# Kernel tuning notes

Measured on AMD Instinct MI355X. Metric: run time of the kernel, lower is better.

## Reference

```python
import jax, jax.numpy as jnp
import numpy as np

B, T, C, H, DH, L, V = 16, 1023, 384, 6, 64, 6, 256
FF = 4 * C
EPS = 1e-5


def _ln(x, g, b):
    mu = x.mean(-1, keepdims=True)
    var = ((x - mu) ** 2).mean(-1, keepdims=True)
    return (x - mu) * jax.lax.rsqrt(var + EPS) * g + b


def setup_inputs() -> dict:
    key = jax.random.key(0)
    ks = jax.random.split(key, 12)
    n = lambda k, shp: jax.random.normal(k, shp, dtype=jnp.float32) * 0.02
    return {
        "x": jax.random.randint(ks[0], (B, T), 0, V),
        "targets": jax.random.randint(ks[1], (B, T), 0, V),
        "tok_emb": n(ks[2], (V, C)),
        "pos_emb": n(ks[3], (T, C)),
        "Wq": n(ks[4], (L, C, C)), "Wk": n(ks[5], (L, C, C)), "Wv": n(ks[6], (L, C, C)),
        "Wo": n(ks[7], (L, C, C)), "bo": jnp.zeros((L, C)),
        "ln1_g": jnp.ones((L, C)), "ln1_b": jnp.zeros((L, C)),
        "ln2_g": jnp.ones((L, C)), "ln2_b": jnp.zeros((L, C)),
        "W1": n(ks[8], (L, C, FF)), "b1": jnp.zeros((L, FF)),
        "W2": n(ks[9], (L, FF, C)), "b2": jnp.zeros((L, C)),
        "lnf_g": jnp.ones((C,)), "lnf_b": jnp.zeros((C,)),
        "Wf": n(ks[10], (C, V)), "bf": jnp.zeros((V,)),
    }


def _forward(x, targets, tok_emb, pos_emb, Wq, Wk, Wv, Wo, bo,
             ln1_g, ln1_b, ln2_g, ln2_b, W1, b1, W2, b2, lnf_g, lnf_b, Wf, bf):
    h = tok_emb[x] + pos_emb[None, :, :]  # [B,T,C]
    tril = jnp.tril(jnp.ones((T, T), bool))

    def heads(z, W):  # [B,T,C] @ [C,C] -> [B,H,T,DH]
        return jnp.einsum('btc,cd->btd', z, W).reshape(B, T, H, DH).transpose(0, 2, 1, 3)

    def layer(h, p):
        wq, wk, wv, wo, bo_, g1, be1, g2, be2, w1, bb1, w2, bb2 = p
        z = _ln(h, g1, be1)
        q, k, v = heads(z, wq), heads(z, wk), heads(z, wv)
        qk = jnp.einsum('bhtd,bhsd->bhts', q, k) * (DH ** -0.5)
        zm = jnp.where(tril, qk, 0.0)
        # faithful to torch: masked_fill_(zeromask == 0, -inf)
        zm = jnp.where(zm == 0.0, -jnp.inf, zm)
        att = jax.nn.softmax(zm, axis=-1)  # dropout = identity (eval)
        o = jnp.einsum('bhts,bhsd->bhtd', att, v).transpose(0, 2, 1, 3).reshape(B, T, C)
        h = h + jnp.einsum('btc,cd->btd', o, wo) + bo_
        z2 = _ln(h, g2, be2)
        ff = jax.nn.relu(jnp.einsum('btc,cf->btf', z2, w1) + bb1)
        h = h + jnp.einsum('btf,fc->btc', ff, w2) + bb2
        return h, None

    params = (Wq, Wk, Wv, Wo, bo, ln1_g, ln1_b, ln2_g, ln2_b, W1, b1, W2, b2)
    h, _ = jax.lax.scan(layer, h, params)
    logits = jnp.einsum('btc,cv->btv', _ln(h, lnf_g, lnf_b), Wf) + bf
    logits2 = logits.reshape(B * T, V)
    logp = jax.nn.log_softmax(logits2, axis=-1)
    loss = -jnp.take_along_axis(logp, targets.reshape(B * T, 1), axis=1).mean()
    return logits2, loss


def reference(x, targets, tok_emb, pos_emb, Wq, Wk, Wv, Wo, bo,
              ln1_g, ln1_b, ln2_g, ln2_b, W1, b1, W2, b2, lnf_g, lnf_b, Wf, bf):
    return _forward(x, targets, tok_emb, pos_emb, Wq, Wk, Wv, Wo, bo,
                    ln1_g, ln1_b, ln2_g, ln2_b, W1, b1, W2, b2, lnf_g, lnf_b, Wf, bf)
```

## Files before the change

kernel.cpp:

```cpp
#include <hip/hip_runtime.h>
#include <hip/hip_bf16.h>
#include <math.h>

#define B_  16
#define T_  1023
#define C_  384
#define H_  6
#define DH_ 64
#define L_  6
#define V_  256
#define FF_ 1536
#define M_  (B_*T_)
#define MP_ 16384
#define EPS_ 1e-5f

typedef __attribute__((ext_vector_type(8))) short bf16x8;
typedef __attribute__((ext_vector_type(4))) short short4v;
typedef __attribute__((ext_vector_type(4))) float f32x4;

__device__ inline short f2bf(float x) {
    union { float f; unsigned u; } c; c.f = x;
    unsigned r = (c.u + 0x7fffu + ((c.u >> 16) & 1u)) >> 16;
    return (short)r;
}

#define GLDS16(g, l) __builtin_amdgcn_global_load_lds(                         \
    (const __attribute__((address_space(1))) void*)(g),                        \
    (__attribute__((address_space(3))) void*)(l), 16, 0, 0)

#define TRRD(dst, va, IMM) asm volatile("ds_read_b64_tr_b16 %0, %1 offset:" IMM \
    : "=v"(dst) : "v"(va))

__global__ void embed_kernel(const int* __restrict__ x, const float* __restrict__ tok,
                             const float* __restrict__ pos, float* __restrict__ h) {
    int i = blockIdx.x * 256 + threadIdx.x;
    if (i >= M_ * C_) return;
    int bt = i / C_;
    int c  = i - bt * C_;
    int t  = bt % T_;
    h[i] = tok[x[bt] * C_ + c] + pos[t * C_ + c];
}

__global__ __launch_bounds__(256) void wconv_kernel(
    const float* __restrict__ Wq, const float* __restrict__ Wk,
    const float* __restrict__ Wv, const float* __restrict__ Wo,
    const float* __restrict__ W1, const float* __restrict__ W2,
    const float* __restrict__ Wf,
    short* __restrict__ qkvt, short* __restrict__ wot, short* __restrict__ w1t,
    short* __restrict__ w2t, short* __restrict__ wft) {
    __shared__ float tile[32][33];
    int t = blockIdx.x;
    const float* src; short* dst; int K, N, tl;
    if (t < 10368) {
        int l = t / 1728, r = t - l * 1728;
        if (r < 432) {
            int which = r / 144; tl = r - which * 144;
            src = (which == 0 ? Wq : which == 1 ? Wk : Wv) + (size_t)l * 384 * 384;
            dst = qkvt + (size_t)l * 1152 * 384 + (size_t)which * 384 * 384;
            K = 384; N = 384;
        } else if (r < 576) {
            tl = r - 432;
            src = Wo + (size_t)l * 384 * 384; dst = wot + (size_t)l * 384 * 384;
            K = 384; N = 384;
        } else if (r < 1152) {
            tl = r - 576;
            src = W1 + (size_t)l * 384 * 1536; dst = w1t + (size_t)l * 1536 * 384;
            K = 384; N = 1536;
        } else {
            tl = r - 1152;
            src = W2 + (size_t)l * 1536 * 384; dst = w2t + (size_t)l * 384 * 1536;
            K = 1536; N = 384;
        }
    } else {
        tl = t - 10368; src = Wf; dst = wft; K = 384; N = 256;
    }
    int ntx = N >> 5;
    int k0 = (tl / ntx) << 5, n0 = (tl % ntx) << 5;
    int rr = threadIdx.x >> 5, cc = threadIdx.x & 31;
#pragma unroll
    for (int p = 0; p < 4; ++p)
        tile[rr + 8 * p][cc] = src[(size_t)(k0 + rr + 8 * p) * N + n0 + cc];
    __syncthreads();
#pragma unroll
    for (int p = 0; p < 4; ++p)
        dst[(size_t)(n0 + rr + 8 * p) * K + k0 + cc] = f2bf(tile[cc][rr + 8 * p]);
}

__global__ __launch_bounds__(256) void ln_kernel(const float* __restrict__ in,
                                                 const float* __restrict__ g,
                                                 const float* __restrict__ b,
                                                 short* __restrict__ out) {
    int wave = threadIdx.x >> 6, lane = threadIdx.x & 63;
    int row  = blockIdx.x * 4 + wave;
    const float* rp = in + (size_t)row * C_;
    float v[6];
    float s = 0.f, s2 = 0.f;
#pragma unroll
    for (int i = 0; i < 6; ++i) {
        v[i] = rp[i * 64 + lane];
        s  += v[i];
        s2 += v[i] * v[i];
    }
#pragma unroll
    for (int o = 32; o > 0; o >>= 1) {
        s  += __shfl_xor(s,  o, 64);
        s2 += __shfl_xor(s2, o, 64);
    }
    float mu  = s * (1.0f / C_);
    float var = s2 * (1.0f / C_) - mu * mu;
    float rs  = rsqrtf(var + EPS_);
    short* op = out + (size_t)row * C_;
#pragma unroll
    for (int i = 0; i < 6; ++i) {
        int c = i * 64 + lane;
        op[c] = f2bf((v[i] - mu) * rs * g[c] + b[c]);
    }
}

template<int MODE, bool RELU, bool HB>
__global__ __launch_bounds__(256) void mm_kernel(const short* __restrict__ A,
                                                 const short* __restrict__ Bt,
                                                 const float* __restrict__ bias,
                                                 short* __restrict__ outb,
                                                 float* __restrict__ outf,
                                                 int N, int K) {
    __shared__ short Al[2][8][128][8];
    __shared__ short Bl[2][8][128][8];
    int tid  = threadIdx.x;
    int wave = tid >> 6, lane = tid & 63;
    int kg4 = lane >> 4, r16 = lane & 15;
    int wr = (wave >> 1) * 64, wc = (wave & 1) * 64;
    int row0 = blockIdx.x * 128, col0 = blockIdx.y * 128;

    const short* ga = A  + (size_t)(row0 + (tid & 127)) * K + ((tid >> 7) << 5);
    const short* gb = Bt + (size_t)(col0 + (tid & 127)) * K + ((tid >> 7) << 5);
    short* alds = &Al[0][0][0][0];
    short* blds = &Bl[0][0][0][0];
    int ldst = ((tid >> 7) << 2) * 1024 + (tid & 127) * 8;

    f32x4 acc[4][4];
#pragma unroll
    for (int i = 0; i < 4; ++i)
#pragma unroll
        for (int j = 0; j < 4; ++j) { acc[i][j][0]=0.f; acc[i][j][1]=0.f; acc[i][j][2]=0.f; acc[i][j][3]=0.f; }

#define MM_STAGE(BUF)                                                          \
    {                                                                          \
        short* la = alds + (BUF) * 8192 + ldst;                                \
        short* lb = blds + (BUF) * 8192 + ldst;                                \
        GLDS16(ga,      la);        GLDS16(ga + 8,  la + 1024);                \
        GLDS16(ga + 16, la + 2048); GLDS16(ga + 24, la + 3072);                \
        GLDS16(gb,      lb);        GLDS16(gb + 8,  lb + 1024);                \
        GLDS16(gb + 16, lb + 2048); GLDS16(gb + 24, lb + 3072);                \
        ga += 64; gb += 64;                                                    \
    }

#define MM_COMPUTE(BUF)                                                        \
    {                                                                          \
        _Pragma("unroll")                                                      \
        for (int p = 0; p < 2; ++p) {                                          \
            const short* ab = alds + (BUF) * 8192 + (4 * p + kg4) * 1024;      \
            const short* bb = blds + (BUF) * 8192 + (4 * p + kg4) * 1024;      \
            bf16x8 av[4], bv[4];                                               \
            _Pragma("unroll")                                                  \
            for (int i = 0; i < 4; ++i) av[i] = *(const bf16x8*)(ab + (wr + 16*i + r16) * 8); \
            _Pragma("unroll")                                                  \
            for (int j = 0; j < 4; ++j) bv[j] = *(const bf16x8*)(bb + (wc + 16*j + r16) * 8); \
            _Pragma("unroll")                                                  \
            for (int i = 0; i < 4; ++i)                                        \
                _Pragma("unroll")                                              \
                for (int j = 0; j < 4; ++j)                                    \
                    acc[i][j] = __builtin_amdgcn_mfma_f32_16x16x32_bf16(av[i], bv[j], acc[i][j], 0, 0, 0); \
        }                                                                      \
    }

    int NT = K >> 6;
    MM_STAGE(0);
    MM_STAGE(1);
    asm volatile("s_waitcnt vmcnt(8)" ::: "memory");
    __builtin_amdgcn_s_barrier();
    asm volatile("" ::: "memory");

    for (int t = 0; t < NT - 1; ++t) {
        MM_COMPUTE(t & 1);
        __builtin_amdgcn_s_barrier();
        asm volatile("" ::: "memory");
        if (t + 2 < NT) {
            MM_STAGE(t & 1);
            asm volatile("s_waitcnt vmcnt(8)" ::: "memory");
        } else {
            asm volatile("s_waitcnt vmcnt(0)" ::: "memory");
        }
        __builtin_amdgcn_s_barrier();
        asm volatile("" ::: "memory");
    }
    MM_COMPUTE((NT - 1) & 1);
#undef MM_STAGE
#undef MM_COMPUTE

#pragma unroll
    for (int j = 0; j < 4; ++j) {
        int col = col0 + wc + 16 * j + r16;
        float bj = HB ? bias[col] : 0.f;
#pragma unroll
        for (int i = 0; i < 4; ++i) {
#pragma unroll
            for (int rg = 0; rg < 4; ++rg) {
                int row = row0 + wr + 16 * i + 4 * kg4 + rg;
                float v = acc[i][j][rg] + bj;
                if (RELU) v = fmaxf(v, 0.f);
                if (MODE == 0) {
                    outb[(size_t)row * N + col] = f2bf(v);
                } else if (MODE == 1) {
                    outf[(size_t)row * N + col] += v;
                } else {
                    if (row < M_) outf[(size_t)row * N + col] = v;
                }
            }
        }
    }
}

__global__ __launch_bounds__(512) void ffn_kernel(const short* zin,
                                                  const short* __restrict__ w1t,
                                                  const short* __restrict__ w2t,
                                                  const float* __restrict__ b1,
                                                  const float* __restrict__ b2,
                                                  float* __restrict__ h,
                                                  const float* __restrict__ lng,
                                                  const float* __restrict__ lnb,
                                                  short* zout) {
    __shared__ short Zl[48 * 64 * 8];
    __shared__ short Pl[16 * 64 * 8];
    int tid  = threadIdx.x;
    int wave = tid >> 6, lane = tid & 63;
    int g = lane >> 4, r16 = lane & 15;
    int r0 = blockIdx.x * 64;

    {
        const short* gz = zin + (size_t)(r0 + lane) * C_ + wave * 8;
        short* lz = Zl + (wave * 64 + lane) * 8;
#pragma unroll
        for (int ro = 0; ro < 6; ++ro) {
            GLDS16(gz, lz);
            gz += 64;
            lz += 8 * 64 * 8;
        }
    }

    const short* w1base = w1t + (size_t)(16 * wave + r16) * C_ + 8 * g;
    const short* w2base = w2t + (size_t)(48 * wave + r16) * FF_ + 8 * g;

    bf16x8 w1f[12];
#pragma unroll
    for (int ks = 0; ks < 12; ++ks)
        w1f[ks] = *(const bf16x8*)(w1base + ks * 32);

    asm volatile("s_waitcnt vmcnt(0)" ::: "memory");
    __builtin_amdgcn_s_barrier();
    asm volatile("" ::: "memory");

    f32x4 acc2[4][3];
#pragma unroll
    for (int mi = 0; mi < 4; ++mi)
#pragma unroll
        for (int j = 0; j < 3; ++j) { acc2[mi][j][0]=0.f; acc2[mi][j][1]=0.f; acc2[mi][j][2]=0.f; acc2[mi][j][3]=0.f; }

    for (int c = 0; c < 12; ++c) {
        bf16x8 w2f[12];
#pragma unroll
        for (int ks2 = 0; ks2 < 4; ++ks2)
#pragma unroll
            for (int j = 0; j < 3; ++j)
                w2f[ks2 * 3 + j] = *(const bf16x8*)(w2base + (size_t)(16 * j) * FF_
                                                    + 128 * c + 32 * ks2);

        f32x4 acc1[4];
#pragma unroll
        for (int mj = 0; mj < 4; ++mj) { acc1[mj][0]=0.f; acc1[mj][1]=0.f; acc1[mj][2]=0.f; acc1[mj][3]=0.f; }
#pragma unroll
        for (int ks = 0; ks < 12; ++ks) {
#pragma unroll
            for (int mj = 0; mj < 4; ++mj) {
                bf16x8 bz = *(const bf16x8*)(Zl + ((4 * ks + g) * 64 + 16 * mj + r16) * 8);
                acc1[mj] = __builtin_amdgcn_mfma_f32_16x16x32_bf16(w1f[ks], bz, acc1[mj], 0, 0, 0);
            }
        }
        f32x4 b1v = *(const f32x4*)(b1 + 128 * c + 16 * wave + 4 * g);
        int oct = 2 * wave + (g >> 1);
#pragma unroll
        for (int mj = 0; mj < 4; ++mj) {
            short4v pv;
#pragma unroll
            for (int rg = 0; rg < 4; ++rg)
                pv[rg] = f2bf(fmaxf(acc1[mj][rg] + b1v[rg], 0.f));
            *(short4v*)(Pl + (oct * 64 + 16 * mj + r16) * 8 + (g & 1) * 4) = pv;
        }
        __syncthreads();

        if (c + 1 < 12) {
#pragma unroll
            for (int ks = 0; ks < 12; ++ks)
                w1f[ks] = *(const bf16x8*)(w1base + (size_t)(c + 1) * 128 * C_ + ks * 32);
        }

#pragma unroll
        for (int ks2 = 0; ks2 < 4; ++ks2) {
            bf16x8 pa[4];
#pragma unroll
            for (int mi = 0; mi < 4; ++mi)
                pa[mi] = *(const bf16x8*)(Pl + ((4 * ks2 + g) * 64 + 16 * mi + r16) * 8);
#pragma unroll
            for (int j = 0; j < 3; ++j) {
#pragma unroll
                for (int mi = 0; mi < 4; ++mi)
                    acc2[mi][j] = __builtin_amdgcn_mfma_f32_16x16x32_bf16(pa[mi], w2f[ks2 * 3 + j], acc2[mi][j], 0, 0, 0);
            }
        }
        __syncthreads();
    }

    float rsum[4][4], rsq[4][4];
#pragma unroll
    for (int mi = 0; mi < 4; ++mi)
#pragma unroll
        for (int rg = 0; rg < 4; ++rg) { rsum[mi][rg] = 0.f; rsq[mi][rg] = 0.f; }

#pragma unroll
    for (int j = 0; j < 3; ++j) {
        int col = 48 * wave + 16 * j + r16;
        float bj = b2[col];
#pragma unroll
        for (int mi = 0; mi < 4; ++mi) {
#pragma unroll
            for (int rg = 0; rg < 4; ++rg) {
                int row = r0 + 16 * mi + 4 * g + rg;
                float hv = h[(size_t)row * C_ + col] + acc2[mi][j][rg] + bj;
                h[(size_t)row * C_ + col] = hv;
                acc2[mi][j][rg] = hv;
                rsum[mi][rg] += hv;
                rsq[mi][rg]  += hv * hv;
            }
        }
    }
#pragma unroll
    for (int o = 1; o < 16; o <<= 1) {
#pragma unroll
        for (int mi = 0; mi < 4; ++mi)
#pragma unroll
            for (int rg = 0; rg < 4; ++rg) {
                rsum[mi][rg] += __shfl_xor(rsum[mi][rg], o, 64);
                rsq[mi][rg]  += __shfl_xor(rsq[mi][rg],  o, 64);
            }
    }
    float* St = (float*)Pl;
    if (r16 == 0) {
#pragma unroll
        for (int mi = 0; mi < 4; ++mi)
#pragma unroll
            for (int rg = 0; rg < 4; ++rg) {
                int rr = 16 * mi + 4 * g + rg;
                St[rr * 16 + 2 * wave]     = rsum[mi][rg];
                St[rr * 16 + 2 * wave + 1] = rsq[mi][rg];
            }
    }
    __syncthreads();
    if (tid < 64) {
        float s = 0.f, s2 = 0.f;
#pragma unroll
        for (int w = 0; w < 8; ++w) { s += St[tid * 16 + 2 * w]; s2 += St[tid * 16 + 2 * w + 1]; }
        float mu  = s * (1.0f / C_);
        float var = s2 * (1.0f / C_) - mu * mu;
        St[tid * 16]     = mu;
        St[tid * 16 + 1] = rsqrtf(var + EPS_);
    }
    __syncthreads();
#pragma unroll
    for (int j = 0; j < 3; ++j) {
        int col = 48 * wave + 16 * j + r16;
        float gam = lng[col], bet = lnb[col];
#pragma unroll
        for (int mi = 0; mi < 4; ++mi) {
#pragma unroll
            for (int rg = 0; rg < 4; ++rg) {
                int rr = 16 * mi + 4 * g + rg;
                float mu = St[rr * 16], rs = St[rr * 16 + 1];
                zout[(size_t)(r0 + rr) * C_ + col] = f2bf((acc2[mi][j][rg] - mu) * rs * gam + bet);
            }
        }
    }
}

__device__ __forceinline__ void attn_step(int kt, int qg, int g, int r16,
                                          const char* Kb, unsigned ka, unsigned va,
                                          short (*Pw)[40],
                                          bf16x8 qf0, bf16x8 qf1,
                                          f32x4* o_acc, float& m, float& l) {
    f32x4 s0, s1;
    s0[0]=0.f;s0[1]=0.f;s0[2]=0.f;s0[3]=0.f;
    s1[0]=0.f;s1[1]=0.f;s1[2]=0.f;s1[3]=0.f;
    bf16x8 a00 = *(const bf16x8*)(Kb + ka);
    bf16x8 a01 = *(const bf16x8*)(Kb + (ka ^ 64u));
    bf16x8 a10 = *(const bf16x8*)(Kb + ka + 2048u);
    bf16x8 a11 = *(const bf16x8*)(Kb + ((ka + 2048u) ^ 64u));
    s0 = __builtin_amdgcn_mfma_f32_16x16x32_bf16(a00, qf0, s0, 0, 0, 0);
    s0 = __builtin_amdgcn_mfma_f32_16x16x32_bf16(a01, qf1, s0, 0, 0, 0);
    s1 = __builtin_amdgcn_mfma_f32_16x16x32_bf16(a10, qf0, s1, 0, 0, 0);
    s1 = __builtin_amdgcn_mfma_f32_16x16x32_bf16(a11, qf1, s1, 0, 0, 0);

    int kb0 = kt * 32 + 4 * g;
    float sv[8];
#pragma unroll
    for (int r = 0; r < 4; ++r) {
        sv[r]     = (kb0 + r      <= qg) ? s0[r] * 0.125f : -3e38f;
        sv[4 + r] = (kb0 + 16 + r <= qg) ? s1[r] * 0.125f : -3e38f;
    }
    float pmax = sv[0];
#pragma unroll
    for (int i = 1; i < 8; ++i) pmax = fmaxf(pmax, sv[i]);
    pmax = fmaxf(pmax, __shfl_xor(pmax, 16, 64));
    pmax = fmaxf(pmax, __shfl_xor(pmax, 32, 64));
    float mn   = fmaxf(m, pmax);
    float corr = __expf(m - mn);
    float rs = 0.f;
    short pb[8];
#pragma unroll
    for (int i = 0; i < 8; ++i) {
        float p = __expf(sv[i] - mn);
        rs += p;
        pb[i] = f2bf(p);
    }
    rs += __shfl_xor(rs, 16, 64);
    rs += __shfl_xor(rs, 32, 64);
    l = l * corr + rs;
    m = mn;

    short4v t0w, t1w;
    t0w[0]=pb[0]; t0w[1]=pb[1]; t0w[2]=pb[2]; t0w[3]=pb[3];
    t1w[0]=pb[4]; t1w[1]=pb[5]; t1w[2]=pb[6]; t1w[3]=pb[7];
    *(short4v*)&Pw[r16][4 * g]      = t0w;
    *(short4v*)&Pw[r16][16 + 4 * g] = t1w;

    short4v v0, v1, v2, v3, v4, v5, v6, v7;
    TRRD(v0, va, "0");    TRRD(v1, va, "512");
    TRRD(v2, va, "128");  TRRD(v3, va, "640");
    TRRD(v4, va, "256");  TRRD(v5, va, "768");
    TRRD(v6, va, "384");  TRRD(v7, va, "896");

    bf16x8 pB = *(const bf16x8*)&Pw[r16][8 * g];
#pragma unroll
    for (int d = 0; d < 4; ++d) {
        o_acc[d][0] *= corr; o_acc[d][1] *= corr;
        o_acc[d][2] *= corr; o_acc[d][3] *= corr;
    }
    asm volatile("s_waitcnt lgkmcnt(0)" ::: "memory");
    __builtin_amdgcn_sched_barrier(0);

    bf16x8 av0, av1, av2, av3;
#pragma unroll
    for (int i = 0; i < 4; ++i) {
        av0[i] = v0[i]; av0[i + 4] = v1[i];
        av1[i] = v2[i]; av1[i + 4] = v3[i];
        av2[i] = v4[i]; av2[i + 4] = v5[i];
        av3[i] = v6[i]; av3[i + 4] = v7[i];
    }
    o_acc[0] = __builtin_amdgcn_mfma_f32_16x16x32_bf16(av0, pB, o_acc[0], 0, 0, 0);
    o_acc[1] = __builtin_amdgcn_mfma_f32_16x16x32_bf16(av1, pB, o_acc[1], 0, 0, 0);
    o_acc[2] = __builtin_amdgcn_mfma_f32_16x16x32_bf16(av2, pB, o_acc[2], 0, 0, 0);
    o_acc[3] = __builtin_amdgcn_mfma_f32_16x16x32_bf16(av3, pB, o_acc[3], 0, 0, 0);
}

__global__ __launch_bounds__(256) void attn_kernel(const short* __restrict__ qkv,
                                                   short* __restrict__ o) {
    __shared__ short Kl[32 * 64];
    __shared__ short Vl[32 * 64];
    __shared__ short P_lds[4][16][40];

    int tid  = threadIdx.x;
    int wave = tid >> 6;
    int lane = tid & 63;
    int g    = lane >> 4;
    int r16  = lane & 15;

    int qtA = blockIdx.x;
    int qtB = 15 - qtA;
    int bh = blockIdx.y;
    int b  = bh / H_, hh = bh - b * H_;
    size_t rbase = (size_t)b * T_;
    int qoff = hh * 64;

    int q0A = qtA * 64, q0B = qtB * 64;
    int qgA = q0A + wave * 16 + r16;
    int qgB = q0B + wave * 16 + r16;

    const short* qrA = qkv + (rbase + qgA) * 1152 + qoff;
    const short* qrB = qkv + (rbase + qgB) * 1152 + qoff;
    bf16x8 qfA0 = *(const bf16x8*)(qrA + 8 * g);
    bf16x8 qfA1 = *(const bf16x8*)(qrA + 32 + 8 * g);
    bf16x8 qfB0 = *(const bf16x8*)(qrB + 8 * g);
    bf16x8 qfB1 = *(const bf16x8*)(qrB + 32 + 8 * g);

    int kkey = tid >> 3;
    int koct = (tid & 7) ^ (kkey & 7);
    const short* gk = qkv + (rbase + kkey) * 1152 + qoff + 384 + koct * 8;
    int vkey = 4 * (tid >> 5) + ((tid >> 1) & 3);
    int voct = 2 * ((tid >> 3) & 3) + (tid & 1);
    const short* gv = qkv + (rbase + vkey) * 1152 + qoff + 768 + voct * 8;
    short* lk = Kl + tid * 8;
    short* lv = Vl + tid * 8;

    f32x4 oA[4], oB[4];
#pragma unroll
    for (int d = 0; d < 4; ++d) {
        oA[d][0]=0.f; oA[d][1]=0.f; oA[d][2]=0.f; oA[d][3]=0.f;
        oB[d][0]=0.f; oB[d][1]=0.f; oB[d][2]=0.f; oB[d][3]=0.f;
    }
    float mA = -3e38f, lA = 0.f, mB = -3e38f, lB = 0.f;

    const char* Kb = (const char*)Kl;
    unsigned ka = (unsigned)(r16 * 128 + ((g ^ (r16 & 7)) << 4));
    unsigned va = (unsigned)(size_t)(__attribute__((address_space(3))) short*)Vl
                + 1024u * (unsigned)g + 8u * (unsigned)r16;

    int ktA_hi = (q0A + wave * 16 + 15) >> 5;
    int ktB_hi = (q0B + wave * 16 + 15) >> 5;
    int nkt = 2 * (qtB + 1);

    for (int kt = 0; kt < nkt; ++kt) {
        __syncthreads();
        GLDS16(gk, lk);
        GLDS16(gv, lv);
        gk += 32 * 1152; gv += 32 * 1152;
        __syncthreads();

        if (kt <= ktB_hi)
            attn_step(kt, qgB, g, r16, Kb, ka, va, P_lds[wave], qfB0, qfB1, oB, mB, lB);
        if (kt <= ktA_hi)
            attn_step(kt, qgA, g, r16, Kb, ka, va, P_lds[wave], qfA0, qfA1, oA, mA, lA);
    }

    {
        float inv = (lA > 0.f) ? 1.f / lA : 0.f;
        short* orow = o + (rbase + qgA) * C_ + qoff;
#pragma unroll
        for (int d = 0; d < 4; ++d) {
            short4v ov;
#pragma unroll
            for (int r = 0; r < 4; ++r) ov[r] = f2bf(oA[d][r] * inv);
            *(short4v*)(orow + 16 * d + 4 * g) = ov;
        }
    }
    if (qgB < T_) {
        float inv = (lB > 0.f) ? 1.f / lB : 0.f;
        short* orow = o + (rbase + qgB) * C_ + qoff;
#pragma unroll
        for (int d = 0; d < 4; ++d) {
            short4v ov;
#pragma unroll
            for (int r = 0; r < 4; ++r) ov[r] = f2bf(oB[d][r] * inv);
            *(short4v*)(orow + 16 * d + 4 * g) = ov;
        }
    }
}

__global__ __launch_bounds__(64) void nll_kernel(const float* __restrict__ logits,
                                                 const int* __restrict__ tgt,
                                                 float* __restrict__ nll) {
    int row  = blockIdx.x;
    int lane = threadIdx.x;
    const float* rp = logits + (size_t)row * V_;
    float v[4];
    float mx = -INFINITY;
#pragma unroll
    for (int i = 0; i < 4; ++i) {
        v[i] = rp[i * 64 + lane];
        mx = fmaxf(mx, v[i]);
    }
#pragma unroll
    for (int o = 32; o > 0; o >>= 1) mx = fmaxf(mx, __shfl_xor(mx, o, 64));
    float s = 0.f;
#pragma unroll
    for (int i = 0; i < 4; ++i) s += expf(v[i] - mx);
#pragma unroll
    for (int o = 32; o > 0; o >>= 1) s += __shfl_xor(s, o, 64);
    if (lane == 0) {
        float lse = mx + logf(s);
        nll[row] = lse - rp[tgt[row]];
    }
}

__global__ __launch_bounds__(256) void loss_kernel(const float* __restrict__ nll,
                                                   float* __restrict__ loss) {
    __shared__ float sm[256];
    float s = 0.f;
    for (int i = threadIdx.x; i < M_; i += 256) s += nll[i];
    sm[threadIdx.x] = s;
    __syncthreads();
    for (int o = 128; o > 0; o >>= 1) {
        if (threadIdx.x < o) sm[threadIdx.x] += sm[threadIdx.x + o];
        __syncthreads();
    }
    if (threadIdx.x == 0) *loss = sm[0] * (1.0f / M_);
}

extern "C" void kernel_launch(void* const* d_in, const int* in_sizes, int n_in,
                              void* d_out, int out_size, void* d_ws, size_t ws_size,
                              hipStream_t stream) {
    const int*   x       = (const int*)d_in[0];
    const int*   targets = (const int*)d_in[1];
    const float* tok_emb = (const float*)d_in[2];
    const float* pos_emb = (const float*)d_in[3];
    const float* Wq      = (const float*)d_in[4];
    const float* Wk      = (const float*)d_in[5];
    const float* Wv      = (const float*)d_in[6];
    const float* Wo      = (const float*)d_in[7];
    const float* bo      = (const float*)d_in[8];
    const float* ln1_g   = (const float*)d_in[9];
    const float* ln1_b   = (const float*)d_in[10];
    const float* ln2_g   = (const float*)d_in[11];
    const float* ln2_b   = (const float*)d_in[12];
    const float* W1      = (const float*)d_in[13];
    const float* b1      = (const float*)d_in[14];
    const float* W2      = (const float*)d_in[15];
    const float* b2      = (const float*)d_in[16];
    const float* lnf_g   = (const float*)d_in[17];
    const float* lnf_b   = (const float*)d_in[18];
    const float* Wf      = (const float*)d_in[19];
    const float* bf      = (const float*)d_in[20];

    float* logits = (float*)d_out;
    float* loss   = logits + (size_t)M_ * V_;

    float* h    = (float*)d_ws;
    short* z    = (short*)(h + (size_t)MP_ * C_);
    short* big  = z + (size_t)MP_ * C_;
    short* ob   = big + (size_t)MP_ * FF_;
    short* qkvt = ob + (size_t)MP_ * C_;
    short* wot  = qkvt + (size_t)L_ * 1152 * 384;
    short* w1t  = wot + (size_t)L_ * 384 * 384;
    short* w2t  = w1t + (size_t)L_ * 1536 * 384;
    short* wft  = w2t + (size_t)L_ * 1536 * 384;
    float* nll  = (float*)(wft + (size_t)256 * 384);

    wconv_kernel<<<10464, 256, 0, stream>>>(Wq, Wk, Wv, Wo, W1, W2, Wf,
                                            qkvt, wot, w1t, w2t, wft);
    embed_kernel<<<(M_ * C_ + 255) / 256, 256, 0, stream>>>(x, tok_emb, pos_emb, h);

    for (int l = 0; l < L_; ++l) {
        if (l == 0)
            ln_kernel<<<M_ / 4, 256, 0, stream>>>(h, ln1_g, ln1_b, z);
        mm_kernel<0, false, false><<<dim3(128, 9), 256, 0, stream>>>(
            z, qkvt + (size_t)l * 1152 * 384, nullptr, big, nullptr, 1152, 384);
        attn_kernel<<<dim3(8, B_ * H_), 256, 0, stream>>>(big, ob);
        mm_kernel<1, false, true><<<dim3(128, 3), 256, 0, stream>>>(
            ob, wot + (size_t)l * 384 * 384, bo + l * C_, nullptr, h, 384, 384);
        ln_kernel<<<M_ / 4, 256, 0, stream>>>(h, ln2_g + l * C_, ln2_b + l * C_, z);
        const float* ng = (l + 1 < L_) ? ln1_g + (l + 1) * C_ : lnf_g;
        const float* nb = (l + 1 < L_) ? ln1_b + (l + 1) * C_ : lnf_b;
        ffn_kernel<<<MP_ / 64, 512, 0, stream>>>(
            z, w1t + (size_t)l * 1536 * 384, w2t + (size_t)l * 384 * 1536,
            b1 + l * FF_, b2 + l * C_, h, ng, nb, z);
    }

    mm_kernel<2, false, true><<<dim3(128, 2), 256, 0, stream>>>(
        z, wft, bf, nullptr, logits, 256, 384);

    nll_kernel<<<M_, 64, 0, stream>>>(logits, targets, nll);
    loss_kernel<<<1, 256, 0, stream>>>(nll, loss);
}
```

Before: 1.323 ms.

## Software-pipeline FFN kernel with double-buffered hidden activations in LDS

Restructures the fused FFN loop so the second GEMM for chunk c runs before the first GEMM for chunk c+1. The hidden activations are double-buffered in shared memory, which removes one of the two barriers per iteration. W1 and W2 weight loads are issued one stage ahead so global latency can overlap MFMA work. It uses twice the LDS for the hidden buffer and may raise register pressure from keeping both weight fragment sets live.

```diff
diff --git a/kernel.cpp b/kernel.cpp
--- a/kernel.cpp
+++ b/kernel.cpp
@@ -231,7 +231,7 @@
                                                   const float* __restrict__ lnb,
                                                   short* zout) {
     __shared__ short Zl[48 * 64 * 8];
-    __shared__ short Pl[16 * 64 * 8];
+    __shared__ short Pl[2][16 * 64 * 8];
     int tid  = threadIdx.x;
     int wave = tid >> 6, lane = tid & 63;
     int g = lane >> 4, r16 = lane & 15;
@@ -251,74 +251,101 @@
     const short* w1base = w1t + (size_t)(16 * wave + r16) * C_ + 8 * g;
     const short* w2base = w2t + (size_t)(48 * wave + r16) * FF_ + 8 * g;
 
-    bf16x8 w1f[12];
-#pragma unroll
-    for (int ks = 0; ks < 12; ++ks)
-        w1f[ks] = *(const bf16x8*)(w1base + ks * 32);
-
+    bf16x8 w1f[12], w2f[12];
+    f32x4 acc1[4];
+    f32x4 acc2[4][3];
+
+#define W1LOAD(cc)                                                             \
+    {                                                                          \
+        _Pragma("unroll")                                                      \
+        for (int ks = 0; ks < 12; ++ks)                                        \
+            w1f[ks] = *(const bf16x8*)(w1base + (size_t)(cc) * 128 * C_ + ks * 32); \
+    }
+
+#define W2LOAD(cc)                                                             \
+    {                                                                          \
+        _Pragma("unroll")                                                      \
+        for (int ks2 = 0; ks2 < 4; ++ks2)                                      \
+            _Pragma("unroll")                                                  \
+            for (int j = 0; j < 3; ++j)                                        \
+                w2f[ks2 * 3 + j] = *(const bf16x8*)(w2base + (size_t)(16 * j) * FF_ \
+                                                    + 128 * (cc) + 32 * ks2);  \
+    }
+
+#define FF1C()                                                                 \
+    {                                                                          \
+        _Pragma("unroll")                                                      \
+        for (int mj = 0; mj < 4; ++mj) { acc1[mj][0]=0.f; acc1[mj][1]=0.f; acc1[mj][2]=0.f; acc1[mj][3]=0.f; } \
+        _Pragma("unroll")                                                      \
+        for (int ks = 0; ks < 12; ++ks)                                        \
+            _Pragma("unroll")                                                  \
+            for (int mj = 0; mj < 4; ++mj) {                                   \
+                bf16x8 bz = *(const bf16x8*)(Zl + ((4 * ks + g) * 64 + 16 * mj + r16) * 8); \
+                acc1[mj] = __builtin_amdgcn_mfma_f32_16x16x32_bf16(w1f[ks], bz, acc1[mj], 0, 0, 0); \
+            }                                                                  \
+    }
+
+#define PSTORE(cc, buf)                                                        \
+    {                                                                          \
+        f32x4 b1v = *(const f32x4*)(b1 + 128 * (cc) + 16 * wave + 4 * g);      \
+        int oct = 2 * wave + (g >> 1);                                         \
+        _Pragma("unroll")                                                      \
+        for (int mj = 0; mj < 4; ++mj) {                                       \
+            short4v pv;                                                        \
+            _Pragma("unroll")                                                  \
+            for (int rg = 0; rg < 4; ++rg)                                     \
+                pv[rg] = f2bf(fmaxf(acc1[mj][rg] + b1v[rg], 0.f));             \
+            *(short4v*)((buf) + (oct * 64 + 16 * mj + r16) * 8 + (g & 1) * 4) = pv; \
+        }                                                                      \
+    }
+
+#define FF2C(buf)                                                              \
+    {                                                                          \
+        _Pragma("unroll")                                                      \
+        for (int ks2 = 0; ks2 < 4; ++ks2) {                                    \
+            bf16x8 pa[4];                                                      \
+            _Pragma("unroll")                                                  \
+            for (int mi = 0; mi < 4; ++mi)                                     \
+                pa[mi] = *(const bf16x8*)((buf) + ((4 * ks2 + g) * 64 + 16 * mi + r16) * 8); \
+            _Pragma("unroll")                                                  \
+            for (int j = 0; j < 3; ++j)                                        \
+                _Pragma("unroll")                                              \
+                for (int mi = 0; mi < 4; ++mi)                                 \
+                    acc2[mi][j] = __builtin_amdgcn_mfma_f32_16x16x32_bf16(pa[mi], w2f[ks2 * 3 + j], acc2[mi][j], 0, 0, 0); \
+        }                                                                      \
+    }
+
+    W1LOAD(0);
     asm volatile("s_waitcnt vmcnt(0)" ::: "memory");
     __builtin_amdgcn_s_barrier();
     asm volatile("" ::: "memory");
 
-    f32x4 acc2[4][3];
 #pragma unroll
     for (int mi = 0; mi < 4; ++mi)
 #pragma unroll
         for (int j = 0; j < 3; ++j) { acc2[mi][j][0]=0.f; acc2[mi][j][1]=0.f; acc2[mi][j][2]=0.f; acc2[mi][j][3]=0.f; }
 
-    for (int c = 0; c < 12; ++c) {
-        bf16x8 w2f[12];
-#pragma unroll
-        for (int ks2 = 0; ks2 < 4; ++ks2)
-#pragma unroll
-            for (int j = 0; j < 3; ++j)
-                w2f[ks2 * 3 + j] = *(const bf16x8*)(w2base + (size_t)(16 * j) * FF_
-                                                    + 128 * c + 32 * ks2);
-
-        f32x4 acc1[4];
-#pragma unroll
-        for (int mj = 0; mj < 4; ++mj) { acc1[mj][0]=0.f; acc1[mj][1]=0.f; acc1[mj][2]=0.f; acc1[mj][3]=0.f; }
-#pragma unroll
-        for (int ks = 0; ks < 12; ++ks) {
-#pragma unroll
-            for (int mj = 0; mj < 4; ++mj) {
-                bf16x8 bz = *(const bf16x8*)(Zl + ((4 * ks + g) * 64 + 16 * mj + r16) * 8);
-                acc1[mj] = __builtin_amdgcn_mfma_f32_16x16x32_bf16(w1f[ks], bz, acc1[mj], 0, 0, 0);
-            }
-        }
-        f32x4 b1v = *(const f32x4*)(b1 + 128 * c + 16 * wave + 4 * g);
-        int oct = 2 * wave + (g >> 1);
-#pragma unroll
-        for (int mj = 0; mj < 4; ++mj) {
-            short4v pv;
-#pragma unroll
-            for (int rg = 0; rg < 4; ++rg)
-                pv[rg] = f2bf(fmaxf(acc1[mj][rg] + b1v[rg], 0.f));
-            *(short4v*)(Pl + (oct * 64 + 16 * mj + r16) * 8 + (g & 1) * 4) = pv;
-        }
+    FF1C();
+    PSTORE(0, Pl[0]);
+    W2LOAD(0);
+    W1LOAD(1);
+    __syncthreads();
+
+    for (int c = 0; c < 11; ++c) {
+        FF2C(Pl[c & 1]);
+        W2LOAD(c + 1);
+        FF1C();
+        if (c + 2 < 12) W1LOAD(c + 2);
+        PSTORE(c + 1, Pl[(c + 1) & 1]);
         __syncthreads();
-
-        if (c + 1 < 12) {
-#pragma unroll
-            for (int ks = 0; ks < 12; ++ks)
-                w1f[ks] = *(const bf16x8*)(w1base + (size_t)(c + 1) * 128 * C_ + ks * 32);
-        }
-
-#pragma unroll
-        for (int ks2 = 0; ks2 < 4; ++ks2) {
-            bf16x8 pa[4];
-#pragma unroll
-            for (int mi = 0; mi < 4; ++mi)
-                pa[mi] = *(const bf16x8*)(Pl + ((4 * ks2 + g) * 64 + 16 * mi + r16) * 8);
-#pragma unroll
-            for (int j = 0; j < 3; ++j) {
-#pragma unroll
-                for (int mi = 0; mi < 4; ++mi)
-                    acc2[mi][j] = __builtin_amdgcn_mfma_f32_16x16x32_bf16(pa[mi], w2f[ks2 * 3 + j], acc2[mi][j], 0, 0, 0);
-            }
-        }
-        __syncthreads();
-    }
+    }
+    FF2C(Pl[1]);
+
+#undef W1LOAD
+#undef W2LOAD
+#undef FF1C
+#undef PSTORE
+#undef FF2C
 
     float rsum[4][4], rsq[4][4];
 #pragma unroll
```

Result: slower. 1.360 ms (+2.8%).

## Add dedicated QKV and Wo+LN2 kernels, move LN1 out of FFN epilogue

Applied to the files above, without the earlier changes.

Replaces the generic mm_kernel for the QKV and Wo projections with 512-thread kernels that stage a 64-row activation tile in LDS and keep weight fragments in registers. The Wo kernel now fuses bias, residual add and LayerNorm2, so the separate LN2 pass goes away. LN1 moves out of the FFN epilogue into a standalone ln_kernel, and the final LN runs separately. nll_kernel now processes four rows per block to cut block count. The aim is to lower GEMM overhead and rebalance fusion, at the cost of keeping one extra LN launch per layer.

```diff
diff --git a/kernel.cpp b/kernel.cpp
--- a/kernel.cpp
+++ b/kernel.cpp
@@ -221,15 +221,198 @@
     }
 }
 
-__global__ __launch_bounds__(512) void ffn_kernel(const short* zin,
+__global__ __launch_bounds__(512) void qkv_kernel(const short* __restrict__ z,
+                                                  const short* __restrict__ wt,
+                                                  short* __restrict__ outb) {
+    __shared__ short Zl[48 * 64 * 8];
+    int tid  = threadIdx.x;
+    int wave = tid >> 6, lane = tid & 63;
+    int g = lane >> 4, r16 = lane & 15;
+    int r0 = blockIdx.x * 64;
+
+    {
+        const short* gz = z + (size_t)(r0 + lane) * C_ + wave * 8;
+        short* lz = Zl + (wave * 64 + lane) * 8;
+#pragma unroll
+        for (int ro = 0; ro < 6; ++ro) { GLDS16(gz, lz); gz += 64; lz += 4096; }
+    }
+
+    const short* wbase = wt + (size_t)(16 * wave + r16) * C_ + 8 * g;
+    bf16x8 wf[12];
+#pragma unroll
+    for (int ks = 0; ks < 12; ++ks) wf[ks] = *(const bf16x8*)(wbase + ks * 32);
+
+    asm volatile("s_waitcnt vmcnt(0)" ::: "memory");
+    __builtin_amdgcn_s_barrier();
+    asm volatile("" ::: "memory");
+
+    for (int c = 0; c < 9; ++c) {
+        f32x4 acc[4];
+#pragma unroll
+        for (int mj = 0; mj < 4; ++mj) { acc[mj][0]=0.f; acc[mj][1]=0.f; acc[mj][2]=0.f; acc[mj][3]=0.f; }
+#pragma unroll
+        for (int ks = 0; ks < 12; ++ks) {
+#pragma unroll
+            for (int mj = 0; mj < 4; ++mj) {
+                bf16x8 bz = *(const bf16x8*)(Zl + ((4 * ks + g) * 64 + 16 * mj + r16) * 8);
+                acc[mj] = __builtin_amdgcn_mfma_f32_16x16x32_bf16(wf[ks], bz, acc[mj], 0, 0, 0);
+            }
+        }
+        if (c + 1 < 9) {
+#pragma unroll
+            for (int ks = 0; ks < 12; ++ks)
+                wf[ks] = *(const bf16x8*)(wbase + (size_t)(c + 1) * 128 * C_ + ks * 32);
+        }
+#pragma unroll
+        for (int mj = 0; mj < 4; ++mj) {
+            short4v ov;
+#pragma unroll
+            for (int rg = 0; rg < 4; ++rg) ov[rg] = f2bf(acc[mj][rg]);
+            *(short4v*)(outb + (size_t)(r0 + 16 * mj + r16) * 1152
+                        + 128 * c + 16 * wave + 4 * g) = ov;
+        }
+    }
+}
+
+__global__ __launch_bounds__(512) void wo_kernel(const short* __restrict__ ob,
+                                                 const short* __restrict__ wt,
+                                                 const float* __restrict__ bo,
+                                                 float* __restrict__ h,
+                                                 const float* __restrict__ lng,
+                                                 const float* __restrict__ lnb,
+                                                 short* __restrict__ zout) {
+    __shared__ short Ol[48 * 64 * 8];
+    int tid  = threadIdx.x;
+    int wave = tid >> 6, lane = tid & 63;
+    int g = lane >> 4, r16 = lane & 15;
+    int r0 = blockIdx.x * 64;
+
+    {
+        const short* go = ob + (size_t)(r0 + lane) * C_ + wave * 8;
+        short* lo = Ol + (wave * 64 + lane) * 8;
+#pragma unroll
+        for (int ro = 0; ro < 6; ++ro) { GLDS16(go, lo); go += 64; lo += 4096; }
+    }
+
+    const short* wbase = wt + (size_t)(48 * wave + r16) * C_ + 8 * g;
+    bf16x8 wf[12];
+#pragma unroll
+    for (int ks2 = 0; ks2 < 4; ++ks2)
+#pragma unroll
+        for (int j = 0; j < 3; ++j)
+            wf[ks2 * 3 + j] = *(const bf16x8*)(wbase + (size_t)(16 * j) * C_ + 32 * ks2);
+
+    asm volatile("s_waitcnt vmcnt(0)" ::: "memory");
+    __builtin_amdgcn_s_barrier();
+    asm volatile("" ::: "memory");
+
+    f32x4 acc[4][3];
+#pragma unroll
+    for (int mi = 0; mi < 4; ++mi)
+#pragma unroll
+        for (int j = 0; j < 3; ++j) { acc[mi][j][0]=0.f; acc[mi][j][1]=0.f; acc[mi][j][2]=0.f; acc[mi][j][3]=0.f; }
+
+    for (int kc = 0; kc < 3; ++kc) {
+#pragma unroll
+        for (int ks2 = 0; ks2 < 4; ++ks2) {
+            bf16x8 pa[4];
+#pragma unroll
+            for (int mi = 0; mi < 4; ++mi)
+                pa[mi] = *(const bf16x8*)(Ol + ((16 * kc + 4 * ks2 + g) * 64 + 16 * mi + r16) * 8);
+#pragma unroll
+            for (int j = 0; j < 3; ++j)
+#pragma unroll
+                for (int mi = 0; mi < 4; ++mi)
+                    acc[mi][j] = __builtin_amdgcn_mfma_f32_16x16x32_bf16(pa[mi], wf[ks2 * 3 + j], acc[mi][j], 0, 0, 0);
+        }
+        if (kc + 1 < 3) {
+#pragma unroll
+            for (int ks2 = 0; ks2 < 4; ++ks2)
+#pragma unroll
+                for (int j = 0; j < 3; ++j)
+                    wf[ks2 * 3 + j] = *(const bf16x8*)(wbase + (size_t)(16 * j) * C_
+                                                       + 128 * (kc + 1) + 32 * ks2);
+        }
+    }
+    __syncthreads();
+
+    float rsum[4][4], rsq[4][4];
+#pragma unroll
+    for (int mi = 0; mi < 4; ++mi)
+#pragma unroll
+        for (int rg = 0; rg < 4; ++rg) { rsum[mi][rg] = 0.f; rsq[mi][rg] = 0.f; }
+
+#pragma unroll
+    for (int j = 0; j < 3; ++j) {
+        int col = 48 * wave + 16 * j + r16;
+        float bj = bo[col];
+#pragma unroll
+        for (int mi = 0; mi < 4; ++mi) {
+#pragma unroll
+            for (int rg = 0; rg < 4; ++rg) {
+                int row = r0 + 16 * mi + 4 * g + rg;
+                float hv = h[(size_t)row * C_ + col] + acc[mi][j][rg] + bj;
+                h[(size_t)row * C_ + col] = hv;
+                acc[mi][j][rg] = hv;
+                rsum[mi][rg] += hv;
+                rsq[mi][rg]  += hv * hv;
+            }
+        }
+    }
+#pragma unroll
+    for (int o = 1; o < 16; o <<= 1) {
+#pragma unroll
+        for (int mi = 0; mi < 4; ++mi)
+#pragma unroll
+            for (int rg = 0; rg < 4; ++rg) {
+                rsum[mi][rg] += __shfl_xor(rsum[mi][rg], o, 64);
+                rsq[mi][rg]  += __shfl_xor(rsq[mi][rg],  o, 64);
+            }
+    }
+    float* St = (float*)Ol;
+    if (r16 == 0) {
+#pragma unroll
+        for (int mi = 0; mi < 4; ++mi)
+#pragma unroll
+            for (int rg = 0; rg < 4; ++rg) {
+                int rr = 16 * mi + 4 * g + rg;
+                St[rr * 16 + 2 * wave]     = rsum[mi][rg];
+                St[rr * 16 + 2 * wave + 1] = rsq[mi][rg];
+            }
+    }
+    __syncthreads();
+    if (tid < 64) {
+        float s = 0.f, s2 = 0.f;
+#pragma unroll
+        for (int w = 0; w < 8; ++w) { s += St[tid * 16 + 2 * w]; s2 += St[tid * 16 + 2 * w + 1]; }
+        float mu  = s * (1.0f / C_);
+        float var = s2 * (1.0f / C_) - mu * mu;
+        St[tid * 16]     = mu;
+        St[tid * 16 + 1] = rsqrtf(var + EPS_);
+    }
+    __syncthreads();
+#pragma unroll
+    for (int j = 0; j < 3; ++j) {
+        int col = 48 * wave + 16 * j + r16;
+        float gam = lng[col], bet = lnb[col];
+#pragma unroll
+        for (int mi = 0; mi < 4; ++mi) {
+#pragma unroll
+            for (int rg = 0; rg < 4; ++rg) {
+                int rr = 16 * mi + 4 * g + rg;
+                float mu = St[rr * 16], rs = St[rr * 16 + 1];
+                zout[(size_t)(r0 + rr) * C_ + col] = f2bf((acc[mi][j][rg] - mu) * rs * gam + bet);
+            }
+        }
+    }
+}
+
+__global__ __launch_bounds__(512) void ffn_kernel(const short* __restrict__ z,
                                                   const short* __restrict__ w1t,
                                                   const short* __restrict__ w2t,
                                                   const float* __restrict__ b1,
                                                   const float* __restrict__ b2,
-                                                  float* __restrict__ h,
-                                                  const float* __restrict__ lng,
-                                                  const float* __restrict__ lnb,
-                                                  short* zout) {
+                                                  float* __restrict__ h) {
     __shared__ short Zl[48 * 64 * 8];
     __shared__ short Pl[16 * 64 * 8];
     int tid  = threadIdx.x;
@@ -238,7 +421,7 @@
     int r0 = blockIdx.x * 64;
 
     {
-        const short* gz = zin + (size_t)(r0 + lane) * C_ + wave * 8;
+        const short* gz = z + (size_t)(r0 + lane) * C_ + wave * 8;
         short* lz = Zl + (wave * 64 + lane) * 8;
 #pragma unroll
         for (int ro = 0; ro < 6; ++ro) {
@@ -320,12 +503,6 @@
         __syncthreads();
     }
 
-    float rsum[4][4], rsq[4][4];
-#pragma unroll
-    for (int mi = 0; mi < 4; ++mi)
-#pragma unroll
-        for (int rg = 0; rg < 4; ++rg) { rsum[mi][rg] = 0.f; rsq[mi][rg] = 0.f; }
-
 #pragma unroll
     for (int j = 0; j < 3; ++j) {
         int col = 48 * wave + 16 * j + r16;
@@ -335,57 +512,7 @@
 #pragma unroll
             for (int rg = 0; rg < 4; ++rg) {
                 int row = r0 + 16 * mi + 4 * g + rg;
-                float hv = h[(size_t)row * C_ + col] + acc2[mi][j][rg] + bj;
-                h[(size_t)row * C_ + col] = hv;
-                acc2[mi][j][rg] = hv;
-                rsum[mi][rg] += hv;
-                rsq[mi][rg]  += hv * hv;
-            }
-        }
-    }
-#pragma unroll
-    for (int o = 1; o < 16; o <<= 1) {
-#pragma unroll
-        for (int mi = 0; mi < 4; ++mi)
-#pragma unroll
-            for (int rg = 0; rg < 4; ++rg) {
-                rsum[mi][rg] += __shfl_xor(rsum[mi][rg], o, 64);
-                rsq[mi][rg]  += __shfl_xor(rsq[mi][rg],  o, 64);
-            }
-    }
-    float* St = (float*)Pl;
-    if (r16 == 0) {
-#pragma unroll
-        for (int mi = 0; mi < 4; ++mi)
-#pragma unroll
-            for (int rg = 0; rg < 4; ++rg) {
-                int rr = 16 * mi + 4 * g + rg;
-                St[rr * 16 + 2 * wave]     = rsum[mi][rg];
-                St[rr * 16 + 2 * wave + 1] = rsq[mi][rg];
-            }
-    }
-    __syncthreads();
-    if (tid < 64) {
-        float s = 0.f, s2 = 0.f;
-#pragma unroll
-        for (int w = 0; w < 8; ++w) { s += St[tid * 16 + 2 * w]; s2 += St[tid * 16 + 2 * w + 1]; }
-        float mu  = s * (1.0f / C_);
-        float var = s2 * (1.0f / C_) - mu * mu;
-        St[tid * 16]     = mu;
-        St[tid * 16 + 1] = rsqrtf(var + EPS_);
-    }
-    __syncthreads();
-#pragma unroll
-    for (int j = 0; j < 3; ++j) {
-        int col = 48 * wave + 16 * j + r16;
-        float gam = lng[col], bet = lnb[col];
-#pragma unroll
-        for (int mi = 0; mi < 4; ++mi) {
-#pragma unroll
-            for (int rg = 0; rg < 4; ++rg) {
-                int rr = 16 * mi + 4 * g + rg;
-                float mu = St[rr * 16], rs = St[rr * 16 + 1];
-                zout[(size_t)(r0 + rr) * C_ + col] = f2bf((acc2[mi][j][rg] - mu) * rs * gam + bet);
+                h[(size_t)row * C_ + col] += acc2[mi][j][rg] + bj;
             }
         }
     }
@@ -563,11 +690,11 @@
     }
 }
 
-__global__ __launch_bounds__(64) void nll_kernel(const float* __restrict__ logits,
-                                                 const int* __restrict__ tgt,
-                                                 float* __restrict__ nll) {
-    int row  = blockIdx.x;
-    int lane = threadIdx.x;
+__global__ __launch_bounds__(256) void nll_kernel(const float* __restrict__ logits,
+                                                  const int* __restrict__ tgt,
+                                                  float* __restrict__ nll) {
+    int wave = threadIdx.x >> 6, lane = threadIdx.x & 63;
+    int row  = blockIdx.x * 4 + wave;
     const float* rp = logits + (size_t)row * V_;
     float v[4];
     float mx = -INFINITY;
@@ -647,24 +774,21 @@
     embed_kernel<<<(M_ * C_ + 255) / 256, 256, 0, stream>>>(x, tok_emb, pos_emb, h);
 
     for (int l = 0; l < L_; ++l) {
-        if (l == 0)
-            ln_kernel<<<M_ / 4, 256, 0, stream>>>(h, ln1_g, ln1_b, z);
-        mm_kernel<0, false, false><<<dim3(128, 9), 256, 0, stream>>>(
-            z, qkvt + (size_t)l * 1152 * 384, nullptr, big, nullptr, 1152, 384);
+        ln_kernel<<<M_ / 4, 256, 0, stream>>>(h, ln1_g + l * C_, ln1_b + l * C_, z);
+        qkv_kernel<<<MP_ / 64, 512, 0, stream>>>(z, qkvt + (size_t)l * 1152 * 384, big);
         attn_kernel<<<dim3(8, B_ * H_), 256, 0, stream>>>(big, ob);
-        mm_kernel<1, false, true><<<dim3(128, 3), 256, 0, stream>>>(
-            ob, wot + (size_t)l * 384 * 384, bo + l * C_, nullptr, h, 384, 384);
-        ln_kernel<<<M_ / 4, 256, 0, stream>>>(h, ln2_g + l * C_, ln2_b + l * C_, z);
-        const float* ng = (l + 1 < L_) ? ln1_g + (l + 1) * C_ : lnf_g;
-        const float* nb = (l + 1 < L_) ? ln1_b + (l + 1) * C_ : lnf_b;
+        wo_kernel<<<MP_ / 64, 512, 0, stream>>>(
+            ob, wot + (size_t)l * 384 * 384, bo + l * C_, h,
+            ln2_g + l * C_, ln2_b + l * C_, z);
         ffn_kernel<<<MP_ / 64, 512, 0, stream>>>(
             z, w1t + (size_t)l * 1536 * 384, w2t + (size_t)l * 384 * 1536,
-            b1 + l * FF_, b2 + l * C_, h, ng, nb, z);
-    }
-
+            b1 + l * FF_, b2 + l * C_, h);
+    }
+
+    ln_kernel<<<M_ / 4, 256, 0, stream>>>(h, lnf_g, lnf_b, z);
     mm_kernel<2, false, true><<<dim3(128, 2), 256, 0, stream>>>(
         z, wft, bf, nullptr, logits, 256, 384);
 
-    nll_kernel<<<M_, 64, 0, stream>>>(logits, targets, nll);
+    nll_kernel<<<M_ / 4, 256, 0, stream>>>(logits, targets, nll);
     loss_kernel<<<1, 256, 0, stream>>>(nll, loss);
 }
```

Measured after the change: 1.275 ms, median of 2. 3.6% less time.
